# Performance work log

Hardware: AMD Instinct MI355X
Metric: run time of the kernel (lower is better)

## Reference

```python
import jax, jax.numpy as jnp
import numpy as np

LOG2 = np.float32(np.log(2.0))

def _jsd_pos(p):
    # get_positive_expectation, measure='JSD', average=False
    return LOG2 - jax.nn.softplus(-p)

def setup_inputs() -> dict:
    key = jax.random.key(0)
    k1, k2, k3, k4, k5, k6 = jax.random.split(key, 6)
    N, G, D = 65536, 512, 256
    batch_1 = jnp.sort(jax.random.randint(k1, (N,), 0, G))
    batch_2 = jnp.sort(jax.random.randint(k2, (N,), 0, G))
    z1 = jax.random.normal(k3, (N, D), dtype=jnp.float32)
    z2 = jax.random.normal(k4, (N, D), dtype=jnp.float32)
    g1 = jax.random.normal(k5, (G, D), dtype=jnp.float32)
    g2 = jax.random.normal(k6, (G, D), dtype=jnp.float32)
    return {"batch_1": batch_1, "batch_2": batch_2, "z1": z1, "z2": z2, "g1": g1, "g2": g2}

def reference(batch_1, batch_2, z1, z2, g1, g2):
    # pos_mask scatter-build -> dense one-hot [N, G]
    pos_mask_1 = jax.nn.one_hot(batch_1, g1.shape[0], dtype=z1.dtype)
    pos_mask_2 = jax.nn.one_hot(batch_2, g2.shape[0], dtype=z2.dtype)
    # masked node-graph similarity matrices [N, G]
    self_sim_1 = (z1 @ g1.T) * pos_mask_1
    self_sim_2 = (z2 @ g2.T) * pos_mask_2
    cross_sim_12 = (z1 @ g2.T) * pos_mask_1
    cross_sim_21 = (z2 @ g1.T) * pos_mask_2
    # sep=True branch: per-node row sums, L2 distance over nodes
    self_js_11 = _jsd_pos(self_sim_1).sum(1)
    cross_js_12 = _jsd_pos(cross_sim_12).sum(1)
    self_js_22 = _jsd_pos(self_sim_2).sum(1)
    cross_js_21 = _jsd_pos(cross_sim_21).sum(1)
    L_1 = jnp.sqrt(jnp.sum((self_js_11 - cross_js_12) ** 2))
    L_2 = jnp.sqrt(jnp.sum((self_js_22 - cross_js_21) ** 2))
    return L_1 + L_2
```

## Files before the change

kernel.cpp:

```cpp
#include <hip/hip_runtime.h>
#include <math.h>

__device__ __forceinline__ float jsd_pos(float p) {
    float sp = fmaxf(-p, 0.0f) + log1pf(expf(-fabsf(p)));
    return 0.69314718055994531f - sp;
}

#define NBLOCKS 2048
#define NODES_PER_WAVE 8

__global__ __launch_bounds__(256) void jsd_dot_kernel(
    const int*   __restrict__ b1,
    const int*   __restrict__ b2,
    const float* __restrict__ z1,
    const float* __restrict__ z2,
    const float* __restrict__ g1,
    const float* __restrict__ g2,
    float*       __restrict__ partials)
{
    const int wave = threadIdx.x >> 6;
    const int lane = threadIdx.x & 63;
    const int w    = blockIdx.x * 4 + wave;

    float acc1 = 0.0f, acc2 = 0.0f;

    #pragma unroll
    for (int j = 0; j < NODES_PER_WAVE; ++j) {
        const int node = w * NODES_PER_WAVE + j;

        const int i1 = b1[node];
        const int i2 = b2[node];

        const float4 a1  = ((const float4*)(z1 + (size_t)node * 256))[lane];
        const float4 a2  = ((const float4*)(z2 + (size_t)node * 256))[lane];
        const float4 w11 = ((const float4*)(g1 + (size_t)i1 * 256))[lane];
        const float4 w12 = ((const float4*)(g2 + (size_t)i1 * 256))[lane];
        const float4 w22 = ((const float4*)(g2 + (size_t)i2 * 256))[lane];
        const float4 w21 = ((const float4*)(g1 + (size_t)i2 * 256))[lane];

        float s11 = a1.x*w11.x + a1.y*w11.y + a1.z*w11.z + a1.w*w11.w;
        float c12 = a1.x*w12.x + a1.y*w12.y + a1.z*w12.z + a1.w*w12.w;
        float s22 = a2.x*w22.x + a2.y*w22.y + a2.z*w22.z + a2.w*w22.w;
        float c21 = a2.x*w21.x + a2.y*w21.y + a2.z*w21.z + a2.w*w21.w;

        #pragma unroll
        for (int off = 32; off >= 1; off >>= 1) {
            s11 += __shfl_down(s11, off, 64);
            c12 += __shfl_down(c12, off, 64);
            s22 += __shfl_down(s22, off, 64);
            c21 += __shfl_down(c21, off, 64);
        }

        if (lane == 0) {
            float d1 = jsd_pos(s11) - jsd_pos(c12);
            float d2 = jsd_pos(s22) - jsd_pos(c21);
            acc1 += d1 * d1;
            acc2 += d2 * d2;
        }
    }

    __shared__ float s1[4], s2[4];
    if (lane == 0) { s1[wave] = acc1; s2[wave] = acc2; }
    __syncthreads();

    if (threadIdx.x == 0) {
        partials[blockIdx.x * 2 + 0] = s1[0] + s1[1] + s1[2] + s1[3];
        partials[blockIdx.x * 2 + 1] = s2[0] + s2[1] + s2[2] + s2[3];
    }
}

__global__ __launch_bounds__(256) void jsd_reduce_kernel(
    const float* __restrict__ partials,
    float*       __restrict__ out)
{
    const int tid  = threadIdx.x;
    const int wave = tid >> 6;
    const int lane = tid & 63;

    float a = 0.0f, b = 0.0f;
    for (int i = tid; i < NBLOCKS; i += 256) {
        a += partials[i * 2 + 0];
        b += partials[i * 2 + 1];
    }

    #pragma unroll
    for (int off = 32; off >= 1; off >>= 1) {
        a += __shfl_down(a, off, 64);
        b += __shfl_down(b, off, 64);
    }

    __shared__ float s1[4], s2[4];
    if (lane == 0) { s1[wave] = a; s2[wave] = b; }
    __syncthreads();

    if (tid == 0) {
        float t1 = s1[0] + s1[1] + s1[2] + s1[3];
        float t2 = s2[0] + s2[1] + s2[2] + s2[3];
        out[0] = sqrtf(t1) + sqrtf(t2);
    }
}

extern "C" void kernel_launch(void* const* d_in, const int* in_sizes, int n_in,
                              void* d_out, int out_size, void* d_ws, size_t ws_size,
                              hipStream_t stream) {
    const int*   b1 = (const int*)  d_in[0];
    const int*   b2 = (const int*)  d_in[1];
    const float* z1 = (const float*)d_in[2];
    const float* z2 = (const float*)d_in[3];
    const float* g1 = (const float*)d_in[4];
    const float* g2 = (const float*)d_in[5];
    float* out      = (float*)d_out;
    float* partials = (float*)d_ws;

    jsd_dot_kernel<<<NBLOCKS, 256, 0, stream>>>(b1, b2, z1, z2, g1, g2, partials);
    jsd_reduce_kernel<<<1, 256, 0, stream>>>(partials, out);
}
```

Baseline: 177.5 us.

## Split each wave into 16-lane groups per node with DPP row reductions

```diff
diff --git a/kernel.cpp b/kernel.cpp
--- a/kernel.cpp
+++ b/kernel.cpp
@@ -1,13 +1,30 @@
 #include <hip/hip_runtime.h>
 #include <math.h>
 
-__device__ __forceinline__ float jsd_pos(float p) {
-    float sp = fmaxf(-p, 0.0f) + log1pf(expf(-fabsf(p)));
-    return 0.69314718055994531f - sp;
+__device__ __forceinline__ float spn(float p) {
+    return fmaxf(-p, 0.0f) + __logf(1.0f + __expf(-fabsf(p)));
+}
+
+__device__ __forceinline__ float dpp_shr_add(float x, float y_unused) { return x; }
+
+__device__ __forceinline__ float row16_reduce(float x) {
+    int xi;
+    xi = __builtin_amdgcn_update_dpp(0, __builtin_bit_cast(int, x), 0x111, 0xf, 0xf, true);
+    x += __builtin_bit_cast(float, xi);
+    xi = __builtin_amdgcn_update_dpp(0, __builtin_bit_cast(int, x), 0x112, 0xf, 0xf, true);
+    x += __builtin_bit_cast(float, xi);
+    xi = __builtin_amdgcn_update_dpp(0, __builtin_bit_cast(int, x), 0x114, 0xf, 0xf, true);
+    x += __builtin_bit_cast(float, xi);
+    xi = __builtin_amdgcn_update_dpp(0, __builtin_bit_cast(int, x), 0x118, 0xf, 0xf, true);
+    x += __builtin_bit_cast(float, xi);
+    return x;
+}
+
+__device__ __forceinline__ float dot4(float4 a, float4 b) {
+    return a.x * b.x + a.y * b.y + a.z * b.z + a.w * b.w;
 }
 
 #define NBLOCKS 2048
-#define NODES_PER_WAVE 8
 
 __global__ __launch_bounds__(256) void jsd_dot_kernel(
     const int*   __restrict__ b1,
@@ -20,52 +37,68 @@
 {
     const int wave = threadIdx.x >> 6;
     const int lane = threadIdx.x & 63;
+    const int q    = lane >> 4;
+    const int lq   = lane & 15;
     const int w    = blockIdx.x * 4 + wave;
 
     float acc1 = 0.0f, acc2 = 0.0f;
 
     #pragma unroll
-    for (int j = 0; j < NODES_PER_WAVE; ++j) {
-        const int node = w * NODES_PER_WAVE + j;
+    for (int g = 0; g < 2; ++g) {
+        const int node = w * 8 + g * 4 + q;
 
         const int i1 = b1[node];
         const int i2 = b2[node];
 
-        const float4 a1  = ((const float4*)(z1 + (size_t)node * 256))[lane];
-        const float4 a2  = ((const float4*)(z2 + (size_t)node * 256))[lane];
-        const float4 w11 = ((const float4*)(g1 + (size_t)i1 * 256))[lane];
-        const float4 w12 = ((const float4*)(g2 + (size_t)i1 * 256))[lane];
-        const float4 w22 = ((const float4*)(g2 + (size_t)i2 * 256))[lane];
-        const float4 w21 = ((const float4*)(g1 + (size_t)i2 * 256))[lane];
+        const float4* z1p  = (const float4*)(z1 + (size_t)node * 256) + lq;
+        const float4* z2p  = (const float4*)(z2 + (size_t)node * 256) + lq;
+        const float4* g11p = (const float4*)(g1 + (size_t)i1 * 256) + lq;
+        const float4* g21p = (const float4*)(g2 + (size_t)i1 * 256) + lq;
+        const float4* g22p = (const float4*)(g2 + (size_t)i2 * 256) + lq;
+        const float4* g12p = (const float4*)(g1 + (size_t)i2 * 256) + lq;
 
-        float s11 = a1.x*w11.x + a1.y*w11.y + a1.z*w11.z + a1.w*w11.w;
-        float c12 = a1.x*w12.x + a1.y*w12.y + a1.z*w12.z + a1.w*w12.w;
-        float s22 = a2.x*w22.x + a2.y*w22.y + a2.z*w22.z + a2.w*w22.w;
-        float c21 = a2.x*w21.x + a2.y*w21.y + a2.z*w21.z + a2.w*w21.w;
+        float s11 = 0.0f, c12 = 0.0f, s22 = 0.0f, c21 = 0.0f;
 
         #pragma unroll
-        for (int off = 32; off >= 1; off >>= 1) {
-            s11 += __shfl_down(s11, off, 64);
-            c12 += __shfl_down(c12, off, 64);
-            s22 += __shfl_down(s22, off, 64);
-            c21 += __shfl_down(c21, off, 64);
+        for (int p = 0; p < 4; ++p) {
+            float4 a1  = z1p[p * 16];
+            float4 a2  = z2p[p * 16];
+            float4 w11 = g11p[p * 16];
+            float4 w12 = g21p[p * 16];
+            float4 w22 = g22p[p * 16];
+            float4 w21 = g12p[p * 16];
+            s11 += dot4(a1, w11);
+            c12 += dot4(a1, w12);
+            s22 += dot4(a2, w22);
+            c21 += dot4(a2, w21);
         }
 
-        if (lane == 0) {
-            float d1 = jsd_pos(s11) - jsd_pos(c12);
-            float d2 = jsd_pos(s22) - jsd_pos(c21);
+        s11 = row16_reduce(s11);
+        c12 = row16_reduce(c12);
+        s22 = row16_reduce(s22);
+        c21 = row16_reduce(c21);
+
+        if (lq == 15) {
+            float d1 = spn(c12) - spn(s11);
+            float d2 = spn(c21) - spn(s22);
             acc1 += d1 * d1;
             acc2 += d2 * d2;
         }
     }
 
-    __shared__ float s1[4], s2[4];
-    if (lane == 0) { s1[wave] = acc1; s2[wave] = acc2; }
+    __shared__ float s1[16], s2[16];
+    if (lq == 15) {
+        s1[wave * 4 + q] = acc1;
+        s2[wave * 4 + q] = acc2;
+    }
     __syncthreads();
 
     if (threadIdx.x == 0) {
-        partials[blockIdx.x * 2 + 0] = s1[0] + s1[1] + s1[2] + s1[3];
-        partials[blockIdx.x * 2 + 1] = s2[0] + s2[1] + s2[2] + s2[3];
+        float t1 = 0.0f, t2 = 0.0f;
+        #pragma unroll
+        for (int i = 0; i < 16; ++i) { t1 += s1[i]; t2 += s2[i]; }
+        partials[blockIdx.x * 2 + 0] = t1;
+        partials[blockIdx.x * 2 + 1] = t2;
     }
 }
 
@@ -78,9 +111,10 @@
     const int lane = tid & 63;
 
     float a = 0.0f, b = 0.0f;
-    for (int i = tid; i < NBLOCKS; i += 256) {
-        a += partials[i * 2 + 0];
-        b += partials[i * 2 + 1];
+    #pragma unroll
+    for (int i = 0; i < NBLOCKS / 256; ++i) {
+        a += partials[(i * 256 + tid) * 2 + 0];
+        b += partials[(i * 256 + tid) * 2 + 1];
     }
 
     #pragma unroll
```

Result: faster. 159.3 us (-10.2%).
